# Kernel tuning notes

Measured on AMD Instinct MI355X. Metric: run time of the kernel, lower is better.

Reference implementation:

```python
import jax, jax.numpy as jnp
import numpy as np

N_NODES = 50000
N_FEAT = 256
N_HID = 256
N_CLASS = 40
N_EDGES = 800000


def setup_inputs() -> dict:
    key = jax.random.key(0)
    ks = jax.random.split(key, 12)
    x = jax.random.normal(ks[0], (N_NODES, N_FEAT), dtype=jnp.float32)
    edge_index = jax.random.randint(ks[1], (2, N_EDGES), 0, N_NODES, dtype=jnp.int64)
    def glorot(k, fan_in, fan_out):
        s = jnp.sqrt(6.0 / (fan_in + fan_out)).astype(jnp.float32)
        return jax.random.uniform(k, (fan_in, fan_out), jnp.float32, -s, s)
    return {
        "x": x,
        "edge_index": edge_index,
        "W1": glorot(ks[2], N_FEAT, N_HID), "b1": jnp.zeros((N_HID,), jnp.float32),
        "W2": glorot(ks[3], N_HID, N_HID), "b2": jnp.zeros((N_HID,), jnp.float32),
        "W3": glorot(ks[4], N_HID, N_HID), "b3": jnp.zeros((N_HID,), jnp.float32),
        "W4": glorot(ks[5], N_HID, N_CLASS), "b4": jnp.zeros((N_CLASS,), jnp.float32),
    }


def _gcn_norm(edge_index, num_nodes):
    # add self-loops, compute symmetric normalization (PyG gcn_norm)
    loop = jnp.arange(num_nodes, dtype=edge_index.dtype)
    src = jnp.concatenate([edge_index[0], loop])
    dst = jnp.concatenate([edge_index[1], loop])
    deg = jax.ops.segment_sum(jnp.ones_like(dst, dtype=jnp.float32), dst,
                              num_segments=num_nodes)
    dis = jnp.where(deg > 0, jax.lax.rsqrt(deg), 0.0)
    norm = dis[src] * dis[dst]  # [E + N]
    return src, dst, norm


def _gcn_conv(x, W, b, src, dst, norm, num_nodes):
    h = x @ W  # dense transform first (out_channels <= in_channels)
    msg = norm[:, None] * h[src]  # gather + scale
    out = jax.ops.segment_sum(msg, dst, num_segments=num_nodes)  # scatter-add
    return out + b


def reference(x, edge_index, W1, b1, W2, b2, W3, b3, W4, b4):
    n = x.shape[0]
    src, dst, norm = _gcn_norm(edge_index, n)
    h = jax.nn.relu(_gcn_conv(x, W1, b1, src, dst, norm, n))
    # dropout is identity in eval mode
    h = jax.nn.relu(_gcn_conv(h, W2, b2, src, dst, norm, n))
    h = jax.nn.relu(_gcn_conv(h, W3, b3, src, dst, norm, n))
    out = _gcn_conv(h, W4, b4, src, dst, norm, n)
    return out
```

## Files before the change

### kernel.cpp

```cpp
#include <hip/hip_runtime.h>

#define NN 50000
#define NF 256
#define NH 256
#define NC 40
#define NE 800000
#define CAP 64

typedef _Float16 f16x8 __attribute__((ext_vector_type(8)));
typedef float f32x4 __attribute__((ext_vector_type(4)));

__device__ __forceinline__ float f16f(unsigned short u) {
  union { unsigned short u; _Float16 h; } a; a.u = u;
  return (float)a.h;
}
__device__ __forceinline__ unsigned short f16u(float f) {
  union { unsigned short u; _Float16 h; } a; a.h = (_Float16)f;
  return a.u;
}

__device__ __forceinline__ void gl16(const void* g, void* l) {
  __builtin_amdgcn_global_load_lds(
      (const __attribute__((address_space(1))) unsigned int*)g,
      (__attribute__((address_space(3))) unsigned int*)l, 16, 0, 0);
}


__global__ void bucket_kernel(const int* __restrict__ src, const int* __restrict__ dst,
                              int* __restrict__ cnt, unsigned short* __restrict__ bucket) {
  int e = blockIdx.x * blockDim.x + threadIdx.x;
  if (e < NE) {
    int d = dst[e], s = src[e];
    int c = atomicAdd(&cnt[d], 1);
    if (c < CAP) bucket[(size_t)d * CAP + c] = (unsigned short)s;
  }
}


__global__ void prep_kernel(const int* __restrict__ cnt, float* __restrict__ dis,
                            const float* __restrict__ W1, const float* __restrict__ W2,
                            const float* __restrict__ W3, const float* __restrict__ W4,
                            unsigned short* __restrict__ Wt1, unsigned short* __restrict__ Wt2,
                            unsigned short* __restrict__ Wt3, unsigned short* __restrict__ Wt4) {
  int idx = blockIdx.x * blockDim.x + threadIdx.x;
  if (idx < 212992) {
    const float* W; unsigned short* Wt; int N;
    if (idx < 65536)       { W = W1; Wt = Wt1; N = 256; }
    else if (idx < 131072) { W = W2; Wt = Wt2; N = 256; idx -= 65536; }
    else if (idx < 196608) { W = W3; Wt = Wt3; N = 256; idx -= 131072; }
    else                   { W = W4; Wt = Wt4; N = 40;  idx -= 196608; }
    int n = idx >> 8, k = idx & 255;
    float v = (n < N) ? W[k * N + n] : 0.0f;
    Wt[idx] = f16u(v);
  } else {
    int i = idx - 212992;
    if (i < NN) dis[i] = rsqrtf((float)(cnt[i] + 1));
  }
}


template <bool AF32>
__global__ __launch_bounds__(256, 4) void gemm_f16(
    const void* __restrict__ Ain, const unsigned short* __restrict__ Bt,
    unsigned short* __restrict__ Cout, int M) {
  __shared__ unsigned short ldsA[64 * 64];
  __shared__ unsigned short ldsB[256 * 64];

  int tid = threadIdx.x;
  int rowBase = blockIdx.x * 64;
  int w = tid >> 6, lane = tid & 63;
  int l15 = lane & 15, l4 = lane >> 4;

  f32x4 acc[4][4] = {};

  for (int kt = 0; kt < 4; ++kt) {
#pragma unroll
    for (int c = 0; c < 2; ++c) {
      int gi = c * 256 + tid;
      int row = gi >> 3, gp = gi & 7;
      int gsrc = gp ^ (row & 7);
      int koff = kt * 64 + gsrc * 8;
      int ar = rowBase + row; ar = ar < M ? ar : M - 1;
      if (AF32) {
        const float* Af = (const float*)Ain + (size_t)ar * 256 + koff;
        float4 v0 = *(const float4*)Af;
        float4 v1 = *(const float4*)(Af + 4);
        f16x8 h = {(_Float16)v0.x, (_Float16)v0.y, (_Float16)v0.z, (_Float16)v0.w,
                   (_Float16)v1.x, (_Float16)v1.y, (_Float16)v1.z, (_Float16)v1.w};
        *(f16x8*)&ldsA[gi * 8] = h;
      } else {
        gl16((const unsigned short*)Ain + (size_t)ar * 256 + koff, &ldsA[gi * 8]);
      }
    }
#pragma unroll
    for (int c = 0; c < 8; ++c) {
      int gi = c * 256 + tid;
      int row = gi >> 3, gp = gi & 7;
      int gsrc = gp ^ (row & 7);
      int koff = kt * 64 + gsrc * 8;
      gl16(Bt + (size_t)row * 256 + koff, &ldsB[gi * 8]);
    }
    __syncthreads();

#pragma unroll
    for (int ks = 0; ks < 2; ++ks) {
      f16x8 a[4], b[4];
      int g = ks * 4 + l4;
#pragma unroll
      for (int mi = 0; mi < 4; ++mi) {
        int arow = mi * 16 + l15;
        int gp = g ^ (arow & 7);
        a[mi] = *(const f16x8*)&ldsA[arow * 64 + gp * 8];
      }
#pragma unroll
      for (int ni = 0; ni < 4; ++ni) {
        int brow = w * 64 + ni * 16 + l15;
        int gp = g ^ (brow & 7);
        b[ni] = *(const f16x8*)&ldsB[brow * 64 + gp * 8];
      }
#pragma unroll
      for (int mi = 0; mi < 4; ++mi)
#pragma unroll
        for (int ni = 0; ni < 4; ++ni)
          acc[mi][ni] = __builtin_amdgcn_mfma_f32_16x16x32_f16(a[mi], b[ni], acc[mi][ni], 0, 0, 0);
    }
    __syncthreads();
  }

#pragma unroll
  for (int ni = 0; ni < 4; ++ni) {
    int col = w * 64 + ni * 16 + l15;
#pragma unroll
    for (int mi = 0; mi < 4; ++mi) {
      f32x4 v = acc[mi][ni];
#pragma unroll
      for (int i = 0; i < 4; ++i) {
        int r = rowBase + mi * 16 + l4 * 4 + i;
        if (r < M) Cout[(size_t)r * 256 + col] = f16u(v[i]);
      }
    }
  }
}


__global__ __launch_bounds__(256) void gemm_n64(
    const unsigned short* __restrict__ A, const unsigned short* __restrict__ Bt,
    unsigned short* __restrict__ Cout, int M) {
  __shared__ unsigned short ldsA[64 * 64];
  __shared__ unsigned short ldsB[64 * 64];

  int tid = threadIdx.x;
  int rowBase = blockIdx.x * 64;
  int w = tid >> 6, lane = tid & 63;
  int l15 = lane & 15, l4 = lane >> 4;

  f32x4 acc[4] = {};

  for (int kt = 0; kt < 4; ++kt) {
#pragma unroll
    for (int c = 0; c < 2; ++c) {
      int gi = c * 256 + tid;
      int row = gi >> 3, gp = gi & 7;
      int gsrc = gp ^ (row & 7);
      int koff = kt * 64 + gsrc * 8;
      int ar = rowBase + row; ar = ar < M ? ar : M - 1;
      gl16(A + (size_t)ar * 256 + koff, &ldsA[gi * 8]);
      gl16(Bt + (size_t)row * 256 + koff, &ldsB[gi * 8]);
    }
    __syncthreads();

#pragma unroll
    for (int ks = 0; ks < 2; ++ks) {
      f16x8 a[4], b;
      int g = ks * 4 + l4;
#pragma unroll
      for (int mi = 0; mi < 4; ++mi) {
        int arow = mi * 16 + l15;
        int gp = g ^ (arow & 7);
        a[mi] = *(const f16x8*)&ldsA[arow * 64 + gp * 8];
      }
      {
        int brow = w * 16 + l15;
        int gp = g ^ (brow & 7);
        b = *(const f16x8*)&ldsB[brow * 64 + gp * 8];
      }
#pragma unroll
      for (int mi = 0; mi < 4; ++mi)
        acc[mi] = __builtin_amdgcn_mfma_f32_16x16x32_f16(a[mi], b, acc[mi], 0, 0, 0);
    }
    __syncthreads();
  }

  int col = w * 16 + l15;
#pragma unroll
  for (int mi = 0; mi < 4; ++mi) {
    f32x4 v = acc[mi];
#pragma unroll
    for (int i = 0; i < 4; ++i) {
      int r = rowBase + mi * 16 + l4 * 4 + i;
      if (r < M) Cout[(size_t)r * 64 + col] = f16u(v[i]);
    }
  }
}


__global__ __launch_bounds__(256) void agg256_kernel(
    const unsigned short* __restrict__ T, unsigned short* __restrict__ P,
    const int* __restrict__ cnt, const unsigned short* __restrict__ bucket,
    const float* __restrict__ dis, const float* __restrict__ b) {
  int node = (blockIdx.x * blockDim.x + threadIdx.x) >> 6;
  int lane = threadIdx.x & 63;
  if (node >= NN) return;
  const ushort4* Tv = (const ushort4*)T;
  float4 bv = ((const float4*)b)[lane];
  float d = dis[node];
  int cv = cnt[node];
  int deg = cv < CAP ? cv : CAP;
  float w0 = d * d;
  ushort4 t = Tv[(size_t)node * 64 + lane];
  float ax = bv.x + w0 * f16f(t.x), ay = bv.y + w0 * f16f(t.y);
  float az = bv.z + w0 * f16f(t.z), aw = bv.w + w0 * f16f(t.w);
  const unsigned short* bk = bucket + (size_t)node * CAP;
  int j = 0;
  for (; j + 4 <= deg; j += 4) {
    int s0 = bk[j], s1 = bk[j + 1], s2 = bk[j + 2], s3 = bk[j + 3];
    ushort4 t0 = Tv[(size_t)s0 * 64 + lane];
    ushort4 t1 = Tv[(size_t)s1 * 64 + lane];
    ushort4 t2 = Tv[(size_t)s2 * 64 + lane];
    ushort4 t3 = Tv[(size_t)s3 * 64 + lane];
    float f0 = d * dis[s0], f1 = d * dis[s1];
    float f2 = d * dis[s2], f3 = d * dis[s3];
    ax += f0 * f16f(t0.x) + f1 * f16f(t1.x) + f2 * f16f(t2.x) + f3 * f16f(t3.x);
    ay += f0 * f16f(t0.y) + f1 * f16f(t1.y) + f2 * f16f(t2.y) + f3 * f16f(t3.y);
    az += f0 * f16f(t0.z) + f1 * f16f(t1.z) + f2 * f16f(t2.z) + f3 * f16f(t3.z);
    aw += f0 * f16f(t0.w) + f1 * f16f(t1.w) + f2 * f16f(t2.w) + f3 * f16f(t3.w);
  }
  for (; j < deg; ++j) {
    int s = bk[j];
    float f = d * dis[s];
    ushort4 ts = Tv[(size_t)s * 64 + lane];
    ax += f * f16f(ts.x); ay += f * f16f(ts.y);
    az += f * f16f(ts.z); aw += f * f16f(ts.w);
  }
  ax = fmaxf(ax, 0.f); ay = fmaxf(ay, 0.f);
  az = fmaxf(az, 0.f); aw = fmaxf(aw, 0.f);
  ushort4 h;
  h.x = f16u(ax); h.y = f16u(ay); h.z = f16u(az); h.w = f16u(aw);
  ((ushort4*)P)[(size_t)node * 64 + lane] = h;
}

__global__ __launch_bounds__(256) void agg40_kernel(
    const unsigned short* __restrict__ T, float* __restrict__ O,
    const int* __restrict__ cnt, const unsigned short* __restrict__ bucket,
    const float* __restrict__ dis, const float* __restrict__ b) {
  int node = (blockIdx.x * blockDim.x + threadIdx.x) >> 6;
  int lane = threadIdx.x & 63;
  if (node >= NN) return;
  float d = dis[node];
  int cv = cnt[node];
  int deg = cv < CAP ? cv : CAP;
  const unsigned short* bk = bucket + (size_t)node * CAP;
  if (lane < NC) {
    float acc = b[lane] + d * d * f16f(T[(size_t)node * 64 + lane]);
    int j = 0;
    for (; j + 4 <= deg; j += 4) {
      int s0 = bk[j], s1 = bk[j + 1], s2 = bk[j + 2], s3 = bk[j + 3];
      float t0 = f16f(T[(size_t)s0 * 64 + lane]);
      float t1 = f16f(T[(size_t)s1 * 64 + lane]);
      float t2 = f16f(T[(size_t)s2 * 64 + lane]);
      float t3 = f16f(T[(size_t)s3 * 64 + lane]);
      acc += d * dis[s0] * t0 + d * dis[s1] * t1 + d * dis[s2] * t2 + d * dis[s3] * t3;
    }
    for (; j < deg; ++j) {
      int s = bk[j];
      acc += d * dis[s] * f16f(T[(size_t)s * 64 + lane]);
    }
    O[(size_t)node * NC + lane] = acc;
  }
}


extern "C" void kernel_launch(void* const* d_in, const int* in_sizes, int n_in,
                              void* d_out, int out_size, void* d_ws, size_t ws_size,
                              hipStream_t stream) {
  const float* x  = (const float*)d_in[0];
  const int* edge = (const int*)d_in[1];
  const float* W1 = (const float*)d_in[2];
  const float* b1 = (const float*)d_in[3];
  const float* W2 = (const float*)d_in[4];
  const float* b2 = (const float*)d_in[5];
  const float* W3 = (const float*)d_in[6];
  const float* b3 = (const float*)d_in[7];
  const float* W4 = (const float*)d_in[8];
  const float* b4 = (const float*)d_in[9];
  float* out = (float*)d_out;

  char* p = (char*)d_ws;
  unsigned short* T16 = (unsigned short*)p; p += (size_t)NN * NH * 2;
  unsigned short* P16 = (unsigned short*)p; p += (size_t)NN * NH * 2;
  int* cnt = (int*)p;                p += (size_t)NN * 4;
  float* dis = (float*)p;            p += (size_t)NN * 4;
  unsigned short* bucket = (unsigned short*)p; p += (size_t)NN * CAP * 2;
  unsigned short* Wt1 = (unsigned short*)p; p += 256 * 256 * 2;
  unsigned short* Wt2 = (unsigned short*)p; p += 256 * 256 * 2;
  unsigned short* Wt3 = (unsigned short*)p; p += 256 * 256 * 2;
  unsigned short* Wt4 = (unsigned short*)p; p += 64 * 256 * 2;

  const int* e_src = edge;
  const int* e_dst = edge + NE;

  hipMemsetAsync(cnt, 0, (size_t)NN * 4, stream);

  bucket_kernel<<<(NE + 255) / 256, 256, 0, stream>>>(e_src, e_dst, cnt, bucket);
  prep_kernel<<<(212992 + NN + 255) / 256, 256, 0, stream>>>(cnt, dis, W1, W2, W3, W4,
                                                             Wt1, Wt2, Wt3, Wt4);

  int gemmBlocks = (NN + 63) / 64;
  int aggBlocks = (NN * 64 + 255) / 256;

  gemm_f16<true><<<gemmBlocks, 256, 0, stream>>>(x, Wt1, T16, NN);
  agg256_kernel<<<aggBlocks, 256, 0, stream>>>(T16, P16, cnt, bucket, dis, b1);
  gemm_f16<false><<<gemmBlocks, 256, 0, stream>>>(P16, Wt2, T16, NN);
  agg256_kernel<<<aggBlocks, 256, 0, stream>>>(T16, P16, cnt, bucket, dis, b2);
  gemm_f16<false><<<gemmBlocks, 256, 0, stream>>>(P16, Wt3, T16, NN);
  agg256_kernel<<<aggBlocks, 256, 0, stream>>>(T16, P16, cnt, bucket, dis, b3);
  gemm_n64<<<gemmBlocks, 256, 0, stream>>>(P16, Wt4, T16, NN);
  agg40_kernel<<<aggBlocks, 256, 0, stream>>>(T16, out, cnt, bucket, dis, b4);
}
```

Baseline: 329.7 us.

## Fuse neighbor aggregation with the next layer's GEMM via an LDS-resident tile

Layers 2–4 now run one kernel each. Each block first gathers and normalizes neighbor features for 64 nodes, applies bias and ReLU, and writes the f16 result into a swizzled LDS tile. It then multiplies that tile by the next weight matrix with MFMA. This removes the global write and re-read of the intermediate aggregated activations and three kernel launches. In exchange, each wave processes 8 nodes serially during the gather phase, and the 64KB LDS footprint limits occupancy, which may reduce latency hiding for the irregular gathers.

New measurement: 362.7 us. +10.0%, slower.

```diff
diff --git a/kernel.cpp b/kernel.cpp
--- a/kernel.cpp
+++ b/kernel.cpp
@@ -59,9 +59,8 @@
 }
 
 
-template <bool AF32>
-__global__ __launch_bounds__(256, 4) void gemm_f16(
-    const void* __restrict__ Ain, const unsigned short* __restrict__ Bt,
+__global__ __launch_bounds__(256, 4) void gemm_l1(
+    const float* __restrict__ Ain, const unsigned short* __restrict__ Bt,
     unsigned short* __restrict__ Cout, int M) {
   __shared__ unsigned short ldsA[64 * 64];
   __shared__ unsigned short ldsB[256 * 64];
@@ -81,16 +80,12 @@
       int gsrc = gp ^ (row & 7);
       int koff = kt * 64 + gsrc * 8;
       int ar = rowBase + row; ar = ar < M ? ar : M - 1;
-      if (AF32) {
-        const float* Af = (const float*)Ain + (size_t)ar * 256 + koff;
-        float4 v0 = *(const float4*)Af;
-        float4 v1 = *(const float4*)(Af + 4);
-        f16x8 h = {(_Float16)v0.x, (_Float16)v0.y, (_Float16)v0.z, (_Float16)v0.w,
-                   (_Float16)v1.x, (_Float16)v1.y, (_Float16)v1.z, (_Float16)v1.w};
-        *(f16x8*)&ldsA[gi * 8] = h;
-      } else {
-        gl16((const unsigned short*)Ain + (size_t)ar * 256 + koff, &ldsA[gi * 8]);
-      }
+      const float* Af = Ain + (size_t)ar * 256 + koff;
+      float4 v0 = *(const float4*)Af;
+      float4 v1 = *(const float4*)(Af + 4);
+      f16x8 h = {(_Float16)v0.x, (_Float16)v0.y, (_Float16)v0.z, (_Float16)v0.w,
+                 (_Float16)v1.x, (_Float16)v1.y, (_Float16)v1.z, (_Float16)v1.w};
+      *(f16x8*)&ldsA[gi * 8] = h;
     }
 #pragma unroll
     for (int c = 0; c < 8; ++c) {
@@ -143,111 +138,121 @@
 }
 
 
-__global__ __launch_bounds__(256) void gemm_n64(
-    const unsigned short* __restrict__ A, const unsigned short* __restrict__ Bt,
-    unsigned short* __restrict__ Cout, int M) {
-  __shared__ unsigned short ldsA[64 * 64];
-  __shared__ unsigned short ldsB[64 * 64];
+template <int NOUT>
+__global__ __launch_bounds__(512, 2) void fused_ag(
+    const unsigned short* __restrict__ Tprev, unsigned short* __restrict__ Tnext,
+    const int* __restrict__ cnt, const unsigned short* __restrict__ bucket,
+    const float* __restrict__ dis, const float* __restrict__ b,
+    const unsigned short* __restrict__ Wt) {
+  __shared__ unsigned short ldsA[64 * 256];
+  __shared__ unsigned short ldsB[NOUT * 64];
 
   int tid = threadIdx.x;
-  int rowBase = blockIdx.x * 64;
-  int w = tid >> 6, lane = tid & 63;
+  int wave = tid >> 6, lane = tid & 63;
+  int nodeBase = blockIdx.x * 64;
+  const ushort4* Tv = (const ushort4*)Tprev;
+  float4 bv = ((const float4*)b)[lane];
+
+  for (int i = 0; i < 8; ++i) {
+    int r = wave * 8 + i;
+    int node = nodeBase + r;
+    if (node < NN) {
+      float d = dis[node];
+      int cv = cnt[node];
+      int deg = cv < CAP ? cv : CAP;
+      float w0 = d * d;
+      ushort4 t = Tv[(size_t)node * 64 + lane];
+      float ax = bv.x + w0 * f16f(t.x), ay = bv.y + w0 * f16f(t.y);
+      float az = bv.z + w0 * f16f(t.z), aw = bv.w + w0 * f16f(t.w);
+      const unsigned short* bk = bucket + (size_t)node * CAP;
+      int j = 0;
+      for (; j + 4 <= deg; j += 4) {
+        int s0 = bk[j], s1 = bk[j + 1], s2 = bk[j + 2], s3 = bk[j + 3];
+        ushort4 t0 = Tv[(size_t)s0 * 64 + lane];
+        ushort4 t1 = Tv[(size_t)s1 * 64 + lane];
+        ushort4 t2 = Tv[(size_t)s2 * 64 + lane];
+        ushort4 t3 = Tv[(size_t)s3 * 64 + lane];
+        float f0 = d * dis[s0], f1 = d * dis[s1];
+        float f2 = d * dis[s2], f3 = d * dis[s3];
+        ax += f0 * f16f(t0.x) + f1 * f16f(t1.x) + f2 * f16f(t2.x) + f3 * f16f(t3.x);
+        ay += f0 * f16f(t0.y) + f1 * f16f(t1.y) + f2 * f16f(t2.y) + f3 * f16f(t3.y);
+        az += f0 * f16f(t0.z) + f1 * f16f(t1.z) + f2 * f16f(t2.z) + f3 * f16f(t3.z);
+        aw += f0 * f16f(t0.w) + f1 * f16f(t1.w) + f2 * f16f(t2.w) + f3 * f16f(t3.w);
+      }
+      for (; j < deg; ++j) {
+        int s = bk[j];
+        float f = d * dis[s];
+        ushort4 ts = Tv[(size_t)s * 64 + lane];
+        ax += f * f16f(ts.x); ay += f * f16f(ts.y);
+        az += f * f16f(ts.z); aw += f * f16f(ts.w);
+      }
+      ax = fmaxf(ax, 0.f); ay = fmaxf(ay, 0.f);
+      az = fmaxf(az, 0.f); aw = fmaxf(aw, 0.f);
+      ushort4 h;
+      h.x = f16u(ax); h.y = f16u(ay); h.z = f16u(az); h.w = f16u(aw);
+      int gp = (lane >> 1) ^ (r & 7);
+      *(ushort4*)&ldsA[r * 256 + gp * 8 + (lane & 1) * 4] = h;
+    }
+  }
+  __syncthreads();
+
+  constexpr int NI = NOUT / 64;
+  int wr = wave >> 2, wc = wave & 3;
   int l15 = lane & 15, l4 = lane >> 4;
-
-  f32x4 acc[4] = {};
+  f32x4 acc[2][NI] = {};
 
   for (int kt = 0; kt < 4; ++kt) {
-#pragma unroll
-    for (int c = 0; c < 2; ++c) {
-      int gi = c * 256 + tid;
+    constexpr int NG = NOUT * 8;
+#pragma unroll
+    for (int c = 0; c < NG / 512; ++c) {
+      int gi = c * 512 + tid;
       int row = gi >> 3, gp = gi & 7;
       int gsrc = gp ^ (row & 7);
-      int koff = kt * 64 + gsrc * 8;
-      int ar = rowBase + row; ar = ar < M ? ar : M - 1;
-      gl16(A + (size_t)ar * 256 + koff, &ldsA[gi * 8]);
-      gl16(Bt + (size_t)row * 256 + koff, &ldsB[gi * 8]);
+      gl16(Wt + (size_t)row * 256 + kt * 64 + gsrc * 8, &ldsB[gi * 8]);
     }
     __syncthreads();
 
 #pragma unroll
     for (int ks = 0; ks < 2; ++ks) {
-      f16x8 a[4], b;
-      int g = ks * 4 + l4;
-#pragma unroll
-      for (int mi = 0; mi < 4; ++mi) {
-        int arow = mi * 16 + l15;
-        int gp = g ^ (arow & 7);
-        a[mi] = *(const f16x8*)&ldsA[arow * 64 + gp * 8];
-      }
-      {
-        int brow = w * 16 + l15;
+      f16x8 a[2], bf[NI];
+#pragma unroll
+      for (int mi = 0; mi < 2; ++mi) {
+        int arow = wr * 32 + mi * 16 + l15;
+        int ga = kt * 8 + ks * 4 + l4;
+        int gp = ga ^ (arow & 7);
+        a[mi] = *(const f16x8*)&ldsA[arow * 256 + gp * 8];
+      }
+#pragma unroll
+      for (int ni = 0; ni < NI; ++ni) {
+        int brow = wc * (NOUT / 4) + ni * 16 + l15;
+        int g = ks * 4 + l4;
         int gp = g ^ (brow & 7);
-        b = *(const f16x8*)&ldsB[brow * 64 + gp * 8];
-      }
-#pragma unroll
-      for (int mi = 0; mi < 4; ++mi)
-        acc[mi] = __builtin_amdgcn_mfma_f32_16x16x32_f16(a[mi], b, acc[mi], 0, 0, 0);
+        bf[ni] = *(const f16x8*)&ldsB[brow * 64 + gp * 8];
+      }
+#pragma unroll
+      for (int mi = 0; mi < 2; ++mi)
+#pragma unroll
+        for (int ni = 0; ni < NI; ++ni)
+          acc[mi][ni] = __builtin_amdgcn_mfma_f32_16x16x32_f16(a[mi], bf[ni], acc[mi][ni], 0, 0, 0);
     }
     __syncthreads();
   }
 
-  int col = w * 16 + l15;
-#pragma unroll
-  for (int mi = 0; mi < 4; ++mi) {
-    f32x4 v = acc[mi];
-#pragma unroll
-    for (int i = 0; i < 4; ++i) {
-      int r = rowBase + mi * 16 + l4 * 4 + i;
-      if (r < M) Cout[(size_t)r * 64 + col] = f16u(v[i]);
-    }
-  }
-}
-
-
-__global__ __launch_bounds__(256) void agg256_kernel(
-    const unsigned short* __restrict__ T, unsigned short* __restrict__ P,
-    const int* __restrict__ cnt, const unsigned short* __restrict__ bucket,
-    const float* __restrict__ dis, const float* __restrict__ b) {
-  int node = (blockIdx.x * blockDim.x + threadIdx.x) >> 6;
-  int lane = threadIdx.x & 63;
-  if (node >= NN) return;
-  const ushort4* Tv = (const ushort4*)T;
-  float4 bv = ((const float4*)b)[lane];
-  float d = dis[node];
-  int cv = cnt[node];
-  int deg = cv < CAP ? cv : CAP;
-  float w0 = d * d;
-  ushort4 t = Tv[(size_t)node * 64 + lane];
-  float ax = bv.x + w0 * f16f(t.x), ay = bv.y + w0 * f16f(t.y);
-  float az = bv.z + w0 * f16f(t.z), aw = bv.w + w0 * f16f(t.w);
-  const unsigned short* bk = bucket + (size_t)node * CAP;
-  int j = 0;
-  for (; j + 4 <= deg; j += 4) {
-    int s0 = bk[j], s1 = bk[j + 1], s2 = bk[j + 2], s3 = bk[j + 3];
-    ushort4 t0 = Tv[(size_t)s0 * 64 + lane];
-    ushort4 t1 = Tv[(size_t)s1 * 64 + lane];
-    ushort4 t2 = Tv[(size_t)s2 * 64 + lane];
-    ushort4 t3 = Tv[(size_t)s3 * 64 + lane];
-    float f0 = d * dis[s0], f1 = d * dis[s1];
-    float f2 = d * dis[s2], f3 = d * dis[s3];
-    ax += f0 * f16f(t0.x) + f1 * f16f(t1.x) + f2 * f16f(t2.x) + f3 * f16f(t3.x);
-    ay += f0 * f16f(t0.y) + f1 * f16f(t1.y) + f2 * f16f(t2.y) + f3 * f16f(t3.y);
-    az += f0 * f16f(t0.z) + f1 * f16f(t1.z) + f2 * f16f(t2.z) + f3 * f16f(t3.z);
-    aw += f0 * f16f(t0.w) + f1 * f16f(t1.w) + f2 * f16f(t2.w) + f3 * f16f(t3.w);
-  }
-  for (; j < deg; ++j) {
-    int s = bk[j];
-    float f = d * dis[s];
-    ushort4 ts = Tv[(size_t)s * 64 + lane];
-    ax += f * f16f(ts.x); ay += f * f16f(ts.y);
-    az += f * f16f(ts.z); aw += f * f16f(ts.w);
-  }
-  ax = fmaxf(ax, 0.f); ay = fmaxf(ay, 0.f);
-  az = fmaxf(az, 0.f); aw = fmaxf(aw, 0.f);
-  ushort4 h;
-  h.x = f16u(ax); h.y = f16u(ay); h.z = f16u(az); h.w = f16u(aw);
-  ((ushort4*)P)[(size_t)node * 64 + lane] = h;
-}
+#pragma unroll
+  for (int ni = 0; ni < NI; ++ni) {
+    int col = wc * (NOUT / 4) + ni * 16 + l15;
+#pragma unroll
+    for (int mi = 0; mi < 2; ++mi) {
+      f32x4 v = acc[mi][ni];
+#pragma unroll
+      for (int i = 0; i < 4; ++i) {
+        int r = nodeBase + wr * 32 + mi * 16 + l4 * 4 + i;
+        if (r < NN) Tnext[(size_t)r * NOUT + col] = f16u(v[i]);
+      }
+    }
+  }
+}
+
 
 __global__ __launch_bounds__(256) void agg40_kernel(
     const unsigned short* __restrict__ T, float* __restrict__ O,
@@ -296,8 +301,8 @@
   float* out = (float*)d_out;
 
   char* p = (char*)d_ws;
-  unsigned short* T16 = (unsigned short*)p; p += (size_t)NN * NH * 2;
-  unsigned short* P16 = (unsigned short*)p; p += (size_t)NN * NH * 2;
+  unsigned short* Ta = (unsigned short*)p; p += (size_t)NN * NH * 2;
+  unsigned short* Tb = (unsigned short*)p; p += (size_t)NN * NH * 2;
   int* cnt = (int*)p;                p += (size_t)NN * 4;
   float* dis = (float*)p;            p += (size_t)NN * 4;
   unsigned short* bucket = (unsigned short*)p; p += (size_t)NN * CAP * 2;
@@ -318,12 +323,9 @@
   int gemmBlocks = (NN + 63) / 64;
   int aggBlocks = (NN * 64 + 255) / 256;
 
-  gemm_f16<true><<<gemmBlocks, 256, 0, stream>>>(x, Wt1, T16, NN);
-  agg256_kernel<<<aggBlocks, 256, 0, stream>>>(T16, P16, cnt, bucket, dis, b1);
-  gemm_f16<false><<<gemmBlocks, 256, 0, stream>>>(P16, Wt2, T16, NN);
-  agg256_kernel<<<aggBlocks, 256, 0, stream>>>(T16, P16, cnt, bucket, dis, b2);
-  gemm_f16<false><<<gemmBlocks, 256, 0, stream>>>(P16, Wt3, T16, NN);
-  agg256_kernel<<<aggBlocks, 256, 0, stream>>>(T16, P16, cnt, bucket, dis, b3);
-  gemm_n64<<<gemmBlocks, 256, 0, stream>>>(P16, Wt4, T16, NN);
-  agg40_kernel<<<aggBlocks, 256, 0, stream>>>(T16, out, cnt, bucket, dis, b4);
-}
+  gemm_l1<<<gemmBlocks, 256, 0, stream>>>(x, Wt1, Ta, NN);
+  fused_ag<256><<<gemmBlocks, 512, 0, stream>>>(Ta, Tb, cnt, bucket, dis, b1, Wt2);
+  fused_ag<256><<<gemmBlocks, 512, 0, stream>>>(Tb, Ta, cnt, bucket, dis, b2, Wt3);
+  fused_ag<64><<<gemmBlocks, 512, 0, stream>>>(Ta, Tb, cnt, bucket, dis, b3, Wt4);
+  agg40_kernel<<<aggBlocks, 256, 0, stream>>>(Tb, out, cnt, bucket, dis, b4);
+}
```
